# Kernel optimization log

Hardware: AMD Instinct MI355X
Metric: run time of the kernel (lower is better)

The kernel has to match this reference:

```python
import jax, jax.numpy as jnp
import numpy as np

BSZ, H, P, L = 8, 512, 128, 8192
DT_MIN, DT_MAX = 1e-3, 1e-1


def setup_inputs() -> dict:
    key = jax.random.key(0)
    ks = jax.random.split(key, 6)
    inp = {}
    inp["input_sequence"] = jax.random.normal(ks[0], (BSZ, 1, H, 1, L), jnp.float32)
    # HiPPO-like init: negative real parts, pi*k imaginary parts
    inp["Lambda_re"] = -jax.random.uniform(ks[1], (P,), jnp.float32, 0.1, 1.0)
    inp["Lambda_im"] = jnp.pi * jnp.arange(P, dtype=jnp.float32)
    # lecun_normal-ish: fan_in = H for B, fan_in = P for C (real+imag parts)
    inp["B"] = jax.random.normal(ks[2], (P, H, 2), jnp.float32) / np.float32(np.sqrt(2 * H))
    inp["C"] = jax.random.normal(ks[3], (H, P, 2), jnp.float32) / np.float32(np.sqrt(2 * P))
    inp["D"] = jax.random.normal(ks[4], (H,), jnp.float32)
    u01 = jax.random.uniform(ks[5], (P, 1), jnp.float32)
    inp["log_step"] = u01 * np.float32(np.log(DT_MAX) - np.log(DT_MIN)) + np.float32(np.log(DT_MIN))
    return inp


def _binary_operator(q_i, q_j):
    A_i, b_i = q_i
    A_j, b_j = q_j
    return (A_j * A_i, A_j * b_i + b_j)


def reference(input_sequence, Lambda_re, Lambda_im, B, C, D, log_step):
    # (bsz, 1, H, 1, L) -> (bsz, L, H)
    u = input_sequence[:, 0, :, 0].transpose(0, 2, 1)

    Lambda = Lambda_re + 1j * Lambda_im                      # (P,)
    B_tilde = B[..., 0] + 1j * B[..., 1]                     # (P, H)
    C_tilde = C[..., 0] + 1j * C[..., 1]                     # (H, P)
    step = jnp.exp(log_step[:, 0])                           # (P,)

    # zero-order hold discretization
    Lambda_bar = jnp.exp(Lambda * step)                      # (P,)
    B_bar = ((Lambda_bar - 1.0) / Lambda)[:, None] * B_tilde # (P, H)

    Bu = jnp.einsum('blh,ph->blp', u, B_bar)                 # (bsz, L, P) complex
    Lambda_elems = jnp.broadcast_to(Lambda_bar, Bu.shape)
    _, xs = jax.lax.associative_scan(_binary_operator, (Lambda_elems, Bu), axis=1)

    # conj_sym=True -> factor of 2 on the real part of emissions
    ys = 2.0 * jnp.einsum('blp,hp->blh', xs, C_tilde).real + D * u
    ys = jax.nn.gelu(ys, approximate=False)

    # back to (bsz, 1, H, 1, L)
    return ys.transpose(0, 2, 1)[:, None, :, None, :]
```

## Files before the change

kernel.cpp:

```cpp
#include <hip/hip_runtime.h>
#include <hip/hip_bf16.h>
#include <cmath>

namespace {
constexpr int Pn = 128;
constexpr int Hn = 512;
constexpr int Ln = 8192;
constexpr int BS = 8;
constexpr size_t HEADB = 525312;
constexpr size_t SZ_BU = (size_t)256 * Ln * 4;
}

typedef __attribute__((ext_vector_type(4))) float f32x4;
typedef __attribute__((ext_vector_type(8))) short bf16x8;

static __device__ inline short f2bf(float x) {
  __hip_bfloat16 h = __float2bfloat16(x);
  return *(short*)&h;
}

static __device__ inline void async_copy16(const void* g, void* l) {
  __builtin_amdgcn_global_load_lds(
      (const __attribute__((address_space(1))) unsigned int*)g,
      (__attribute__((address_space(3))) unsigned int*)l, 16, 0, 0);
}

__global__ void precompute_kernel(const float* __restrict__ Lre,
                                  const float* __restrict__ Lim,
                                  const float* __restrict__ Bin,
                                  const float* __restrict__ Cin,
                                  const float* __restrict__ lstep,
                                  float* __restrict__ Lam,
                                  __hip_bfloat16* __restrict__ Bmat,
                                  __hip_bfloat16* __restrict__ Cmat) {
  int tid = blockIdx.x * blockDim.x + threadIdx.x;
  if (tid < 2 * Pn * Hn) {
    int r = tid >> 9;
    int h = tid & (Hn - 1);
    int p = r & (Pn - 1);
    float st = expf(lstep[p]);
    float lr = Lre[p], li = Lim[p];
    float er = expf(lr * st);
    float cr = er * cosf(li * st);
    float ci = er * sinf(li * st);
    float nr = cr - 1.0f, ni = ci;
    float inv = 1.0f / (lr * lr + li * li);
    float wr = (nr * lr + ni * li) * inv;
    float wi = (ni * lr - nr * li) * inv;
    float btr = Bin[(p * Hn + h) * 2 + 0];
    float bti = Bin[(p * Hn + h) * 2 + 1];
    float val = (r < Pn) ? (wr * btr - wi * bti) : (wr * bti + wi * btr);
    Bmat[tid] = __float2bfloat16(val);
  } else if (tid < 4 * Pn * Hn) {
    int j = tid - 2 * Pn * Hn;
    int h = j >> 8;
    int c = j & 255;
    int p = c & (Pn - 1);
    float v = (c < Pn) ? 2.0f * Cin[(h * Pn + p) * 2 + 0]
                       : -2.0f * Cin[(h * Pn + p) * 2 + 1];
    Cmat[j] = __float2bfloat16(v);
  } else if (tid < 4 * Pn * Hn + 256) {
    int j = tid - 4 * Pn * Hn;
    int p = j & (Pn - 1);
    float st = expf(lstep[p]);
    float lr = Lre[p], li = Lim[p];
    float er = expf(lr * st);
    Lam[j] = (j < Pn) ? er * cosf(li * st) : er * sinf(li * st);
  }
}

__global__ __launch_bounds__(256) void gemm1_kernel(
    const __hip_bfloat16* __restrict__ Amat,
    const float* __restrict__ U,
    float* __restrict__ Bu,
    int b0) {
  __shared__ __align__(16) short As[128 * 32];
  __shared__ __align__(16) short Bs[128 * 40];
  const int t = threadIdx.x;
  const int lane = t & 63, w = t >> 6;
  const int wm = w >> 1, wn = w & 1;
  const int n0 = blockIdx.x * 128;
  const int m0 = blockIdx.y * 128;
  const int bz = blockIdx.z;
  const float* Ub = U + (size_t)(b0 + bz) * Hn * Ln;

  const int srow = lane >> 2, scol = (lane & 3) * 16;
  const int bn = t & 127, bkg = t >> 7;

  f32x4 acc[4][4] = {};
  for (int k0 = 0; k0 < Hn; k0 += 32) {
#pragma unroll
    for (int I2 = 0; I2 < 2; I2++) {
      int I = 2 * w + I2;
      async_copy16((const char*)(Amat + (size_t)(m0 + 16 * I + srow) * Hn + k0) + scol,
                   (char*)As + I * 1024);
    }
#pragma unroll
    for (int p = 0; p < 2; p++) {
      int kb = p * 16 + bkg * 8;
      float v[8];
#pragma unroll
      for (int j = 0; j < 8; j++)
        v[j] = Ub[(size_t)(k0 + kb + j) * Ln + n0 + bn];
      bf16x8 pk;
#pragma unroll
      for (int j = 0; j < 8; j++) pk[j] = f2bf(v[j]);
      *(bf16x8*)&Bs[bn * 40 + kb] = pk;
    }
    __syncthreads();
    bf16x8 af[4], bfr[4];
#pragma unroll
    for (int mt = 0; mt < 4; mt++)
      af[mt] = *(const bf16x8*)&As[(64 * wm + 16 * mt + (lane & 15)) * 32 + (lane >> 4) * 8];
#pragma unroll
    for (int nt = 0; nt < 4; nt++)
      bfr[nt] = *(const bf16x8*)&Bs[(64 * wn + 16 * nt + (lane & 15)) * 40 + (lane >> 4) * 8];
#pragma unroll
    for (int mt = 0; mt < 4; mt++)
#pragma unroll
      for (int nt = 0; nt < 4; nt++)
        acc[mt][nt] = __builtin_amdgcn_mfma_f32_16x16x32_bf16(
            af[mt], bfr[nt], acc[mt][nt], 0, 0, 0);
    __syncthreads();
  }
  const int row4 = (lane >> 4) * 4, col = lane & 15;
  float* Bub = Bu + (size_t)bz * 256 * Ln;
#pragma unroll
  for (int mt = 0; mt < 4; mt++)
#pragma unroll
    for (int nt = 0; nt < 4; nt++) {
      int n = n0 + 64 * wn + 16 * nt + col;
#pragma unroll
      for (int r = 0; r < 4; r++) {
        int m = m0 + 64 * wm + 16 * mt + row4 + r;
        Bub[(size_t)m * Ln + n] = acc[mt][nt][r];
      }
    }
}

__global__ __launch_bounds__(256) void scan_kernel(float* __restrict__ Bu,
                                                   const float* __restrict__ Lam) {
  const int p = blockIdx.x;
  const int bz = blockIdx.y;
  const float Ar = Lam[p], Ai = Lam[Pn + p];
  float* rre = Bu + ((size_t)bz * 256 + p) * Ln;
  float* rim = Bu + ((size_t)bz * 256 + Pn + p) * Ln;
  const int t = threadIdx.x;
  const int l0 = t * 32;

  float br[32], bi[32];
  const float4* pr = (const float4*)(rre + l0);
  const float4* pi = (const float4*)(rim + l0);
#pragma unroll
  for (int i = 0; i < 8; i++) {
    float4 v = pr[i];
    br[4 * i] = v.x; br[4 * i + 1] = v.y; br[4 * i + 2] = v.z; br[4 * i + 3] = v.w;
  }
#pragma unroll
  for (int i = 0; i < 8; i++) {
    float4 v = pi[i];
    bi[4 * i] = v.x; bi[4 * i + 1] = v.y; bi[4 * i + 2] = v.z; bi[4 * i + 3] = v.w;
  }

  float xr = 0.f, xi = 0.f;
#pragma unroll
  for (int j = 0; j < 32; j++) {
    float nr = fmaf(Ar, xr, fmaf(-Ai, xi, br[j]));
    float ni = fmaf(Ar, xi, fmaf(Ai, xr, bi[j]));
    xr = nr; xi = ni;
  }
  float ar = Ar, ai = Ai;
#pragma unroll
  for (int s = 0; s < 5; s++) {
    float trr = ar * ar - ai * ai;
    float tii = 2.0f * ar * ai;
    ar = trr; ai = tii;
  }

  __shared__ float sar[256], sai[256], sbr[256], sbi[256];
  sar[t] = ar; sai[t] = ai; sbr[t] = xr; sbi[t] = xi;
  for (int off = 1; off < 256; off <<= 1) {
    __syncthreads();
    float par = 0.f, pai = 0.f, pbr = 0.f, pbi = 0.f;
    float car = 0.f, cai = 0.f, cbr = 0.f, cbi = 0.f;
    if (t >= off) {
      par = sar[t - off]; pai = sai[t - off];
      pbr = sbr[t - off]; pbi = sbi[t - off];
      car = sar[t]; cai = sai[t]; cbr = sbr[t]; cbi = sbi[t];
    }
    __syncthreads();
    if (t >= off) {
      sbr[t] = cbr + car * pbr - cai * pbi;
      sbi[t] = cbi + car * pbi + cai * pbr;
      sar[t] = car * par - cai * pai;
      sai[t] = car * pai + cai * par;
    }
  }
  __syncthreads();
  float cr = (t > 0) ? sbr[t - 1] : 0.f;
  float ci = (t > 0) ? sbi[t - 1] : 0.f;

  xr = cr; xi = ci;
  float4* qr = (float4*)(rre + l0);
  float4* qi = (float4*)(rim + l0);
#pragma unroll
  for (int i = 0; i < 8; i++) {
    float4 vr, vi;
#pragma unroll
    for (int c = 0; c < 4; c++) {
      float nr = fmaf(Ar, xr, fmaf(-Ai, xi, br[4 * i + c]));
      float ni = fmaf(Ar, xi, fmaf(Ai, xr, bi[4 * i + c]));
      xr = nr; xi = ni;
      (&vr.x)[c] = xr;
      (&vi.x)[c] = xi;
    }
    qr[i] = vr;
    qi[i] = vi;
  }
}

__global__ __launch_bounds__(256) void gemm2_kernel(
    const __hip_bfloat16* __restrict__ Cmat,
    const float* __restrict__ Xs,
    const float* __restrict__ U,
    const float* __restrict__ Dv,
    float* __restrict__ Out, int b0) {
  __shared__ __align__(16) short As[128 * 32];
  __shared__ __align__(16) short Bs[128 * 40];
  const int t = threadIdx.x;
  const int lane = t & 63, w = t >> 6;
  const int wm = w >> 1, wn = w & 1;
  const int n0 = blockIdx.x * 128;
  const int m0 = blockIdx.y * 128;
  const int bz = blockIdx.z;
  const int b = b0 + bz;
  const float* Xb = Xs + (size_t)bz * 256 * Ln;

  const int srow = lane >> 2, scol = (lane & 3) * 16;
  const int bn = t & 127, bkg = t >> 7;

  f32x4 acc[4][4] = {};
  for (int k0 = 0; k0 < 256; k0 += 32) {
#pragma unroll
    for (int I2 = 0; I2 < 2; I2++) {
      int I = 2 * w + I2;
      async_copy16((const char*)(Cmat + (size_t)(m0 + 16 * I + srow) * 256 + k0) + scol,
                   (char*)As + I * 1024);
    }
#pragma unroll
    for (int p = 0; p < 2; p++) {
      int kb = p * 16 + bkg * 8;
      float v[8];
#pragma unroll
      for (int j = 0; j < 8; j++)
        v[j] = Xb[(size_t)(k0 + kb + j) * Ln + n0 + bn];
      bf16x8 pk;
#pragma unroll
      for (int j = 0; j < 8; j++) pk[j] = f2bf(v[j]);
      *(bf16x8*)&Bs[bn * 40 + kb] = pk;
    }
    __syncthreads();
    bf16x8 af[4], bfr[4];
#pragma unroll
    for (int mt = 0; mt < 4; mt++)
      af[mt] = *(const bf16x8*)&As[(64 * wm + 16 * mt + (lane & 15)) * 32 + (lane >> 4) * 8];
#pragma unroll
    for (int nt = 0; nt < 4; nt++)
      bfr[nt] = *(const bf16x8*)&Bs[(64 * wn + 16 * nt + (lane & 15)) * 40 + (lane >> 4) * 8];
#pragma unroll
    for (int mt = 0; mt < 4; mt++)
#pragma unroll
      for (int nt = 0; nt < 4; nt++)
        acc[mt][nt] = __builtin_amdgcn_mfma_f32_16x16x32_bf16(
            af[mt], bfr[nt], acc[mt][nt], 0, 0, 0);
    __syncthreads();
  }
  const int row4 = (lane >> 4) * 4, col = lane & 15;
#pragma unroll
  for (int mt = 0; mt < 4; mt++) {
#pragma unroll
    for (int r = 0; r < 4; r++) {
      int h = m0 + 64 * wm + 16 * mt + row4 + r;
      float dh = Dv[h];
      const float* Urow = U + ((size_t)b * Hn + h) * Ln;
      float* Orow = Out + ((size_t)b * Hn + h) * Ln;
#pragma unroll
      for (int nt = 0; nt < 4; nt++) {
        int n = n0 + 64 * wn + 16 * nt + col;
        float y = acc[mt][nt][r] + dh * Urow[n];
        float u2 = y * (0.7978845608f + 0.0356774081f * y * y);
        Orow[n] = y / (1.0f + __expf(-2.0f * u2));
      }
    }
  }
}

extern "C" void kernel_launch(void* const* d_in, const int* in_sizes, int n_in,
                              void* d_out, int out_size, void* d_ws, size_t ws_size,
                              hipStream_t stream) {
  const float* U   = (const float*)d_in[0];
  const float* Lre = (const float*)d_in[1];
  const float* Lim = (const float*)d_in[2];
  const float* Bin = (const float*)d_in[3];
  const float* Cin = (const float*)d_in[4];
  const float* Dv  = (const float*)d_in[5];
  const float* ls  = (const float*)d_in[6];
  float* out = (float*)d_out;

  char* wsb = (char*)d_ws;
  float* Lam = (float*)wsb;
  __hip_bfloat16* Bmat = (__hip_bfloat16*)(wsb + 1024);
  __hip_bfloat16* Cmat = (__hip_bfloat16*)(wsb + 263168);

  int NB = 8;
  while (NB > 1 && ws_size < HEADB + (size_t)NB * SZ_BU)
    NB >>= 1;
  float* Bu = (float*)(wsb + HEADB);

  precompute_kernel<<<(4 * Pn * Hn + 256 + 255) / 256, 256, 0, stream>>>(
      Lre, Lim, Bin, Cin, ls, Lam, Bmat, Cmat);

  for (int b0 = 0; b0 < BS; b0 += NB) {
    gemm1_kernel<<<dim3(Ln / 128, 2, NB), 256, 0, stream>>>(Bmat, U, Bu, b0);
    scan_kernel<<<dim3(Pn, NB), 256, 0, stream>>>(Bu, Lam);
    gemm2_kernel<<<dim3(Ln / 128, Hn / 128, NB), 256, 0, stream>>>(
        Cmat, Bu, U, Dv, out, b0);
  }
}
```

Measured before the change: 359.6 us.

## Store Bu time-major and split scan into chunk-ends, carry, and apply passes

Transposes the Bu/Xs intermediate from state-major (p, L) to time-major (L, 256) so gemm1 writes vectorized f32x4 and gemm2 reads contiguous float4 rows along k. The single-block-per-state scan is replaced by three kernels: per-32-step chunk end states, a sequential carry propagation across 256 chunks using a precomputed Lambda^32, and an apply pass that rescans each chunk from its carry. This removes the shared-memory Hillis-Steele scan and its many barriers, but adds two extra launches, reads Bu twice, and puts a serial 256-step carry kernel with only NB blocks on the critical path.

```diff
diff --git a/kernel.cpp b/kernel.cpp
--- a/kernel.cpp
+++ b/kernel.cpp
@@ -7,7 +7,11 @@
 constexpr int Hn = 512;
 constexpr int Ln = 8192;
 constexpr int BS = 8;
-constexpr size_t HEADB = 525312;
+constexpr size_t OFF_BMAT = 2048;
+constexpr size_t OFF_CMAT = 264192;
+constexpr size_t OFF_END  = 526336;
+constexpr size_t OFF_CAR  = 2623488;
+constexpr size_t HEADB    = 4720640;
 constexpr size_t SZ_BU = (size_t)256 * Ln * 4;
 }
 
@@ -59,13 +63,16 @@
     float v = (c < Pn) ? 2.0f * Cin[(h * Pn + p) * 2 + 0]
                        : -2.0f * Cin[(h * Pn + p) * 2 + 1];
     Cmat[j] = __float2bfloat16(v);
-  } else if (tid < 4 * Pn * Hn + 256) {
+  } else if (tid < 4 * Pn * Hn + 512) {
     int j = tid - 4 * Pn * Hn;
-    int p = j & (Pn - 1);
+    int p = j & 127;
+    int sel = j >> 7;
     float st = expf(lstep[p]);
     float lr = Lre[p], li = Lim[p];
-    float er = expf(lr * st);
-    Lam[j] = (j < Pn) ? er * cosf(li * st) : er * sinf(li * st);
+    float sc = (sel < 2) ? st : 32.0f * st;
+    float er = expf(lr * sc);
+    Lam[(sel >> 1) * 256 + (sel & 1) * 128 + p] =
+        (sel & 1) ? er * sinf(li * sc) : er * cosf(li * sc);
   }
 }
 
@@ -124,98 +131,114 @@
     __syncthreads();
   }
   const int row4 = (lane >> 4) * 4, col = lane & 15;
-  float* Bub = Bu + (size_t)bz * 256 * Ln;
+  float* Bub = Bu + (size_t)bz * Ln * 256;
 #pragma unroll
   for (int mt = 0; mt < 4; mt++)
 #pragma unroll
     for (int nt = 0; nt < 4; nt++) {
       int n = n0 + 64 * wn + 16 * nt + col;
-#pragma unroll
-      for (int r = 0; r < 4; r++) {
-        int m = m0 + 64 * wm + 16 * mt + row4 + r;
-        Bub[(size_t)m * Ln + n] = acc[mt][nt][r];
+      int m = m0 + 64 * wm + 16 * mt + row4;
+      *(f32x4*)&Bub[(size_t)n * 256 + m] = acc[mt][nt];
+    }
+}
+
+__global__ __launch_bounds__(256) void scan_ends_kernel(const float* __restrict__ Bu,
+                                                        const float* __restrict__ Lam,
+                                                        float* __restrict__ End) {
+  const int bz = blockIdx.y;
+  const int t = threadIdx.x;
+  const int c = blockIdx.x * 2 + (t >> 7);
+  const int p = t & 127;
+  const float Ar = Lam[p], Ai = Lam[128 + p];
+  const float* base = Bu + ((size_t)bz * Ln + (size_t)c * 32) * 256;
+  float br[32], bi[32];
+#pragma unroll
+  for (int i = 0; i < 32; i++) br[i] = base[(size_t)i * 256 + p];
+#pragma unroll
+  for (int i = 0; i < 32; i++) bi[i] = base[(size_t)i * 256 + 128 + p];
+  float xr = 0.f, xi = 0.f;
+#pragma unroll
+  for (int i = 0; i < 32; i++) {
+    float nr = fmaf(Ar, xr, fmaf(-Ai, xi, br[i]));
+    float ni = fmaf(Ar, xi, fmaf(Ai, xr, bi[i]));
+    xr = nr; xi = ni;
+  }
+  float* E = End + ((size_t)bz * 256 + c) * 256;
+  E[p] = xr;
+  E[128 + p] = xi;
+}
+
+__global__ __launch_bounds__(128) void carry_kernel(const float* __restrict__ End,
+                                                    float* __restrict__ Carry,
+                                                    const float* __restrict__ Lam) {
+  const int bz = blockIdx.x;
+  const int p = threadIdx.x;
+  const float a32r = Lam[256 + p], a32i = Lam[384 + p];
+  const float* E = End + (size_t)bz * 256 * 256;
+  float* C = Carry + (size_t)bz * 256 * 256;
+  float xr = 0.f, xi = 0.f;
+  float er0[4], ei0[4], er1[4], ei1[4];
+#pragma unroll
+  for (int q = 0; q < 4; q++) {
+    er0[q] = E[(size_t)q * 256 + p];
+    ei0[q] = E[(size_t)q * 256 + 128 + p];
+  }
+  for (int c0 = 0; c0 < 256; c0 += 8) {
+#pragma unroll
+    for (int q = 0; q < 4; q++) {
+      er1[q] = E[(size_t)(c0 + 4 + q) * 256 + p];
+      ei1[q] = E[(size_t)(c0 + 4 + q) * 256 + 128 + p];
+    }
+#pragma unroll
+    for (int q = 0; q < 4; q++) {
+      C[(size_t)(c0 + q) * 256 + p] = xr;
+      C[(size_t)(c0 + q) * 256 + 128 + p] = xi;
+      float nr = fmaf(a32r, xr, fmaf(-a32i, xi, er0[q]));
+      float ni = fmaf(a32r, xi, fmaf(a32i, xr, ei0[q]));
+      xr = nr; xi = ni;
+    }
+#pragma unroll
+    for (int q = 0; q < 4; q++) {
+      int cn = c0 + 8 + q;
+      if (cn < 256) {
+        er0[q] = E[(size_t)cn * 256 + p];
+        ei0[q] = E[(size_t)cn * 256 + 128 + p];
       }
     }
-}
-
-__global__ __launch_bounds__(256) void scan_kernel(float* __restrict__ Bu,
-                                                   const float* __restrict__ Lam) {
-  const int p = blockIdx.x;
+#pragma unroll
+    for (int q = 0; q < 4; q++) {
+      C[(size_t)(c0 + 4 + q) * 256 + p] = xr;
+      C[(size_t)(c0 + 4 + q) * 256 + 128 + p] = xi;
+      float nr = fmaf(a32r, xr, fmaf(-a32i, xi, er1[q]));
+      float ni = fmaf(a32r, xi, fmaf(a32i, xr, ei1[q]));
+      xr = nr; xi = ni;
+    }
+  }
+}
+
+__global__ __launch_bounds__(256) void scan_apply_kernel(float* __restrict__ Bu,
+                                                         const float* __restrict__ Lam,
+                                                         const float* __restrict__ Carry) {
   const int bz = blockIdx.y;
-  const float Ar = Lam[p], Ai = Lam[Pn + p];
-  float* rre = Bu + ((size_t)bz * 256 + p) * Ln;
-  float* rim = Bu + ((size_t)bz * 256 + Pn + p) * Ln;
   const int t = threadIdx.x;
-  const int l0 = t * 32;
-
+  const int c = blockIdx.x * 2 + (t >> 7);
+  const int p = t & 127;
+  const float Ar = Lam[p], Ai = Lam[128 + p];
+  float* base = Bu + ((size_t)bz * Ln + (size_t)c * 32) * 256;
+  const float* Cg = Carry + ((size_t)bz * 256 + c) * 256;
   float br[32], bi[32];
-  const float4* pr = (const float4*)(rre + l0);
-  const float4* pi = (const float4*)(rim + l0);
-#pragma unroll
-  for (int i = 0; i < 8; i++) {
-    float4 v = pr[i];
-    br[4 * i] = v.x; br[4 * i + 1] = v.y; br[4 * i + 2] = v.z; br[4 * i + 3] = v.w;
-  }
-#pragma unroll
-  for (int i = 0; i < 8; i++) {
-    float4 v = pi[i];
-    bi[4 * i] = v.x; bi[4 * i + 1] = v.y; bi[4 * i + 2] = v.z; bi[4 * i + 3] = v.w;
-  }
-
-  float xr = 0.f, xi = 0.f;
-#pragma unroll
-  for (int j = 0; j < 32; j++) {
-    float nr = fmaf(Ar, xr, fmaf(-Ai, xi, br[j]));
-    float ni = fmaf(Ar, xi, fmaf(Ai, xr, bi[j]));
+#pragma unroll
+  for (int i = 0; i < 32; i++) br[i] = base[(size_t)i * 256 + p];
+#pragma unroll
+  for (int i = 0; i < 32; i++) bi[i] = base[(size_t)i * 256 + 128 + p];
+  float xr = Cg[p], xi = Cg[128 + p];
+#pragma unroll
+  for (int i = 0; i < 32; i++) {
+    float nr = fmaf(Ar, xr, fmaf(-Ai, xi, br[i]));
+    float ni = fmaf(Ar, xi, fmaf(Ai, xr, bi[i]));
     xr = nr; xi = ni;
-  }
-  float ar = Ar, ai = Ai;
-#pragma unroll
-  for (int s = 0; s < 5; s++) {
-    float trr = ar * ar - ai * ai;
-    float tii = 2.0f * ar * ai;
-    ar = trr; ai = tii;
-  }
-
-  __shared__ float sar[256], sai[256], sbr[256], sbi[256];
-  sar[t] = ar; sai[t] = ai; sbr[t] = xr; sbi[t] = xi;
-  for (int off = 1; off < 256; off <<= 1) {
-    __syncthreads();
-    float par = 0.f, pai = 0.f, pbr = 0.f, pbi = 0.f;
-    float car = 0.f, cai = 0.f, cbr = 0.f, cbi = 0.f;
-    if (t >= off) {
-      par = sar[t - off]; pai = sai[t - off];
-      pbr = sbr[t - off]; pbi = sbi[t - off];
-      car = sar[t]; cai = sai[t]; cbr = sbr[t]; cbi = sbi[t];
-    }
-    __syncthreads();
-    if (t >= off) {
-      sbr[t] = cbr + car * pbr - cai * pbi;
-      sbi[t] = cbi + car * pbi + cai * pbr;
-      sar[t] = car * par - cai * pai;
-      sai[t] = car * pai + cai * par;
-    }
-  }
-  __syncthreads();
-  float cr = (t > 0) ? sbr[t - 1] : 0.f;
-  float ci = (t > 0) ? sbi[t - 1] : 0.f;
-
-  xr = cr; xi = ci;
-  float4* qr = (float4*)(rre + l0);
-  float4* qi = (float4*)(rim + l0);
-#pragma unroll
-  for (int i = 0; i < 8; i++) {
-    float4 vr, vi;
-#pragma unroll
-    for (int c = 0; c < 4; c++) {
-      float nr = fmaf(Ar, xr, fmaf(-Ai, xi, br[4 * i + c]));
-      float ni = fmaf(Ar, xi, fmaf(Ai, xr, bi[4 * i + c]));
-      xr = nr; xi = ni;
-      (&vr.x)[c] = xr;
-      (&vi.x)[c] = xi;
-    }
-    qr[i] = vr;
-    qi[i] = vi;
+    base[(size_t)i * 256 + p] = nr;
+    base[(size_t)i * 256 + 128 + p] = ni;
   }
 }
 
@@ -234,10 +257,10 @@
   const int m0 = blockIdx.y * 128;
   const int bz = blockIdx.z;
   const int b = b0 + bz;
-  const float* Xb = Xs + (size_t)bz * 256 * Ln;
 
   const int srow = lane >> 2, scol = (lane & 3) * 16;
   const int bn = t & 127, bkg = t >> 7;
+  const float* Xrow = Xs + ((size_t)bz * Ln + n0 + bn) * 256;
 
   f32x4 acc[4][4] = {};
   for (int k0 = 0; k0 < 256; k0 += 32) {
@@ -248,15 +271,13 @@
                    (char*)As + I * 1024);
     }
 #pragma unroll
-    for (int p = 0; p < 2; p++) {
-      int kb = p * 16 + bkg * 8;
-      float v[8];
-#pragma unroll
-      for (int j = 0; j < 8; j++)
-        v[j] = Xb[(size_t)(k0 + kb + j) * Ln + n0 + bn];
+    for (int p2 = 0; p2 < 2; p2++) {
+      int kb = p2 * 16 + bkg * 8;
+      f32x4 x0 = *(const f32x4*)&Xrow[k0 + kb];
+      f32x4 x1 = *(const f32x4*)&Xrow[k0 + kb + 4];
       bf16x8 pk;
 #pragma unroll
-      for (int j = 0; j < 8; j++) pk[j] = f2bf(v[j]);
+      for (int q = 0; q < 4; q++) { pk[q] = f2bf(x0[q]); pk[4 + q] = f2bf(x1[q]); }
       *(bf16x8*)&Bs[bn * 40 + kb] = pk;
     }
     __syncthreads();
@@ -309,20 +330,24 @@
 
   char* wsb = (char*)d_ws;
   float* Lam = (float*)wsb;
-  __hip_bfloat16* Bmat = (__hip_bfloat16*)(wsb + 1024);
-  __hip_bfloat16* Cmat = (__hip_bfloat16*)(wsb + 263168);
+  __hip_bfloat16* Bmat = (__hip_bfloat16*)(wsb + OFF_BMAT);
+  __hip_bfloat16* Cmat = (__hip_bfloat16*)(wsb + OFF_CMAT);
+  float* End = (float*)(wsb + OFF_END);
+  float* Cy  = (float*)(wsb + OFF_CAR);
+  float* Bu  = (float*)(wsb + HEADB);
 
   int NB = 8;
   while (NB > 1 && ws_size < HEADB + (size_t)NB * SZ_BU)
     NB >>= 1;
-  float* Bu = (float*)(wsb + HEADB);
-
-  precompute_kernel<<<(4 * Pn * Hn + 256 + 255) / 256, 256, 0, stream>>>(
+
+  precompute_kernel<<<(4 * Pn * Hn + 512 + 255) / 256, 256, 0, stream>>>(
       Lre, Lim, Bin, Cin, ls, Lam, Bmat, Cmat);
 
   for (int b0 = 0; b0 < BS; b0 += NB) {
     gemm1_kernel<<<dim3(Ln / 128, 2, NB), 256, 0, stream>>>(Bmat, U, Bu, b0);
-    scan_kernel<<<dim3(Pn, NB), 256, 0, stream>>>(Bu, Lam);
+    scan_ends_kernel<<<dim3(128, NB), 256, 0, stream>>>(Bu, Lam, End);
+    carry_kernel<<<dim3(NB), 128, 0, stream>>>(End, Cy, Lam);
+    scan_apply_kernel<<<dim3(128, NB), 256, 0, stream>>>(Bu, Lam, Cy);
     gemm2_kernel<<<dim3(Ln / 128, Hn / 128, NB), 256, 0, stream>>>(
         Cmat, Bu, U, Dv, out, b0);
   }
```

After: 376.8 us. +4.8%, slower.
